# Optimization experiments

Hardware: AMD Instinct MI355X
Metric: run time of the kernel (lower is better)

## Reference

```python
import jax, jax.numpy as jnp
import numpy as np

DIM, HEADS, HD, FFN = 1536, 12, 128, 8960
B, F, H, W = 1, 4, 20, 32
S = F * H * W          # 2560 latent tokens
L2 = 512               # text context length
EPS = 1e-6


def _ln(x):
    m = jnp.mean(x, -1, keepdims=True)
    v = jnp.mean(jnp.square(x - m), -1, keepdims=True)
    return (x - m) * jax.lax.rsqrt(v + EPS)


def _rms(x, g):
    return x * jax.lax.rsqrt(jnp.mean(jnp.square(x), -1, keepdims=True) + EPS) * g


def _dyn_quant(x):
    # per-token symmetric int8 dynamic activation quantization (A8, dynamic input scale)
    s = jnp.maximum(jnp.max(jnp.abs(x), -1, keepdims=True) / 127.0, 1e-8)
    q = jnp.clip(jnp.round(x / s), -127.0, 127.0)
    return q, s, jnp.sum(q, -1)   # sum_input used for asymmetric-weight zero-point correction


def _quant_w(w):
    # per-output-channel asymmetric int8 weight quantization (weight_sym=False)
    wmin = jnp.min(w, 1, keepdims=True)
    wmax = jnp.max(w, 1, keepdims=True)
    s = jnp.maximum((wmax - wmin) / 255.0, 1e-8)
    zp = jnp.round(-128.0 - wmin / s)
    qw = jnp.clip(jnp.round(w / s) + zp, -128.0, 127.0)
    return qw, s[:, 0], zp[:, 0]


def _w8a8(qx, s_x, sum_qx, w, b):
    # y = s_x * s_w * (qx @ (qw - zp)^T) + b = s_x*s_w*(qx@qw^T - zp*sum(qx)) + b
    qw, sw, zp = _quant_w(w)
    acc = jnp.einsum('bsi,oi->bso', qx, qw) - sum_qx[..., None] * zp
    return acc * s_x * sw + b


def _rope(x, fr, f, h, w):
    # x: [B,S,N,D] with S == f*h*w; fr: [1024, D//2] complex rope table
    Bn, Sn, N, D = x.shape
    c = D // 2
    s0 = c - 2 * (c // 3)
    fF = jnp.broadcast_to(fr[:f, :s0].reshape(f, 1, 1, s0), (f, h, w, s0))
    fH = jnp.broadcast_to(fr[:h, s0:s0 + c // 3].reshape(1, h, 1, c // 3), (f, h, w, c // 3))
    fW = jnp.broadcast_to(fr[:w, s0 + c // 3:].reshape(1, 1, w, c // 3), (f, h, w, c // 3))
    fi = jnp.concatenate([fF, fH, fW], -1).reshape(1, f * h * w, 1, c)
    xr = x.reshape(Bn, Sn, N, c, 2)
    xc = jax.lax.complex(xr[..., 0], xr[..., 1]) * fi
    return jnp.stack([jnp.real(xc), jnp.imag(xc)], -1).reshape(Bn, Sn, N, D)


def _attn(q, k, v, k_lens):
    scale = 1.0 / jnp.sqrt(jnp.float32(q.shape[-1]))
    scores = jnp.einsum('bqnd,bknd->bnqk', q, k) * scale
    mask = jnp.arange(k.shape[1])[None, None, None, :] < k_lens[:, None, None, None]
    p = jax.nn.softmax(jnp.where(mask, scores, -1e30), -1)
    return jnp.einsum('bnqk,bknd->bqnd', p, v)


def _forward(x, e, freqs, context, modulation,
             wq, bq, wk, bk, wv, bv, wo, bo, gq, gk, n3_w, n3_b,
             cwq, cbq, cwk, cbk, cwv, cbv, cwo, cbo, cgq, cgk,
             w1, b1, w2, b2, f, h, w, seq_lens, context_lens):
    fr = jax.lax.complex(freqs[..., 0], freqs[..., 1])
    em = modulation + e  # [B,6,C]
    sm, sc, gm, smlp, scmlp, gmlp = [em[:, i:i + 1] for i in range(6)]
    Bn, Sn, C = x.shape
    # --- self attention: fused norm+modulation then shared per-token int8 quant for q/k/v ---
    h1 = _ln(x) * (1.0 + sc) + sm
    qx, s_x, sum_qx = _dyn_quant(h1)
    q = _rms(_w8a8(qx, s_x, sum_qx, wq, bq), gq).reshape(Bn, Sn, HEADS, HD)
    k = _rms(_w8a8(qx, s_x, sum_qx, wk, bk), gk).reshape(Bn, Sn, HEADS, HD)
    v = _w8a8(qx, s_x, sum_qx, wv, bv).reshape(Bn, Sn, HEADS, HD)
    q = _rope(q, fr, f, h, w)
    k = _rope(k, fr, f, h, w)
    y = _attn(q, k, v, seq_lens).reshape(Bn, Sn, C) @ wo.T + bo
    x = x + y * gm
    # --- cross attention (fp16/fp path in the original; use_kernel[1]=False) ---
    hx = _ln(x) * n3_w + n3_b
    cq = _rms(hx @ cwq.T + cbq, cgq).reshape(Bn, Sn, HEADS, HD)
    ck = _rms(context @ cwk.T + cbk, cgk).reshape(Bn, L2, HEADS, HD)
    cv = (context @ cwv.T + cbv).reshape(Bn, L2, HEADS, HD)
    y = _attn(cq, ck, cv, context_lens).reshape(Bn, Sn, C) @ cwo.T + cbo
    x = x + y
    # --- FFN with modulation (use_kernel[2]=False) ---
    h2 = _ln(x) * (1.0 + scmlp) + smlp
    y = jax.nn.gelu(h2 @ w1.T + b1, approximate=True) @ w2.T + b2
    return x + y * gmlp


def setup_inputs():
    key = jax.random.key(0)
    ks = jax.random.split(key, 16)

    def P(i, shape, s=0.02):
        return jax.random.normal(ks[i], shape, jnp.float32) * s

    x = jax.random.normal(ks[0], (B, S, DIM), jnp.float32)
    e = jax.random.normal(ks[1], (B, 6, DIM), jnp.float32)
    context = jax.random.normal(ks[2], (B, L2, DIM), jnp.float32)
    seq_lens = jnp.array([S], jnp.int32)
    grid_sizes = jnp.array([[F, H, W]], jnp.int32)
    context_lens = jnp.array([L2], jnp.int32)
    c = HD // 2
    pos = np.arange(1024, dtype=np.float64)[:, None]
    theta = 1.0 / (10000.0 ** (np.arange(c, dtype=np.float64) / c))
    ang = pos * theta
    freqs = jnp.asarray(np.stack([np.cos(ang), np.sin(ang)], -1), jnp.float32)
    z = lambda n: jnp.zeros((n,), jnp.float32)
    o = lambda n: jnp.ones((n,), jnp.float32)
    return dict(x=x, e=e, seq_lens=seq_lens, grid_sizes=grid_sizes, freqs=freqs,
                context=context, context_lens=context_lens,
                modulation=P(3, (1, 6, DIM), 1.0 / DIM ** 0.5),
                wq=P(4, (DIM, DIM)), bq=z(DIM), wk=P(5, (DIM, DIM)), bk=z(DIM),
                wv=P(6, (DIM, DIM)), bv=z(DIM), wo=P(7, (DIM, DIM)), bo=z(DIM),
                gq=o(DIM), gk=o(DIM), n3_w=o(DIM), n3_b=z(DIM),
                cwq=P(8, (DIM, DIM)), cbq=z(DIM), cwk=P(9, (DIM, DIM)), cbk=z(DIM),
                cwv=P(10, (DIM, DIM)), cbv=z(DIM), cwo=P(11, (DIM, DIM)), cbo=z(DIM),
                cgq=o(DIM), cgk=o(DIM),
                w1=P(12, (FFN, DIM)), b1=z(FFN), w2=P(13, (DIM, FFN)), b2=z(DIM))


def reference(x, e, seq_lens, grid_sizes, freqs, context, context_lens, modulation,
              wq, bq, wk, bk, wv, bv, wo, bo, gq, gk, n3_w, n3_b,
              cwq, cbq, cwk, cbk, cwv, cbv, cwo, cbo, cgq, cgk,
              w1, b1, w2, b2):
    f, h, w = int(grid_sizes[0, 0]), int(grid_sizes[0, 1]), int(grid_sizes[0, 2])
    return _forward(x, e, freqs, context, modulation,
                    wq, bq, wk, bk, wv, bv, wo, bo, gq, gk, n3_w, n3_b,
                    cwq, cbq, cwk, cbk, cwv, cbv, cwo, cbo, cgq, cgk,
                    w1, b1, w2, b2, f, h, w, seq_lens, context_lens)
```

## Files before the change

### kernel.cpp

```cpp
#include <hip/hip_runtime.h>
#include <stdint.h>


typedef unsigned short u16;
typedef __bf16 bf16x8 __attribute__((ext_vector_type(8)));
typedef float f32x4 __attribute__((ext_vector_type(4)));

#define DEV __device__ __forceinline__

DEV u16 f2b(float f) {
  uint32_t u = __float_as_uint(f);
  u += 0x7fffu + ((u >> 16) & 1u);
  return (u16)(u >> 16);
}

DEV float gelu_tanh(float v) {
  float u = 0.7978845608028654f * (v + 0.044715f * v * v * v);
  return 0.5f * v * (1.0f + tanhf(u));
}

DEV void gl_lds16(const u16* g, u16* l) {
  __builtin_amdgcn_global_load_lds(
      (const __attribute__((address_space(1))) void*)g,
      (__attribute__((address_space(3))) void*)l, 16, 0, 0);
}

DEV float bred_sum(float v, float* scr) {
  #pragma unroll
  for (int o = 32; o; o >>= 1) v += __shfl_down(v, o, 64);
  if ((threadIdx.x & 63) == 0) scr[threadIdx.x >> 6] = v;
  __syncthreads();
  v = scr[0] + scr[1] + scr[2] + scr[3];
  __syncthreads();
  return v;
}
DEV float bred_max(float v, float* scr) {
  #pragma unroll
  for (int o = 32; o; o >>= 1) v = fmaxf(v, __shfl_down(v, o, 64));
  if ((threadIdx.x & 63) == 0) scr[threadIdx.x >> 6] = v;
  __syncthreads();
  v = fmaxf(fmaxf(scr[0], scr[1]), fmaxf(scr[2], scr[3]));
  __syncthreads();
  return v;
}
DEV float bred_min(float v, float* scr) {
  #pragma unroll
  for (int o = 32; o; o >>= 1) v = fminf(v, __shfl_down(v, o, 64));
  if ((threadIdx.x & 63) == 0) scr[threadIdx.x >> 6] = v;
  __syncthreads();
  v = fminf(fminf(scr[0], scr[1]), fminf(scr[2], scr[3]));
  __syncthreads();
  return v;
}

__global__ __launch_bounds__(256) void pack_kernel(
    const float* __restrict__ e, const float* __restrict__ mod,
    const float* __restrict__ cbk, const float* __restrict__ cbv,
    float* __restrict__ em, float* __restrict__ bckv) {
  int i = blockIdx.x * 256 + threadIdx.x;
  if (i < 9216) em[i] = e[i] + mod[i];
  if (i < 3072) bckv[i] = (i < 1536) ? cbk[i] : cbv[i - 1536];
}

__global__ __launch_bounds__(256) void cvt_bf16_kernel(
    const float* __restrict__ in, u16* __restrict__ out, int n4) {
  int stride = gridDim.x * 256;
  for (int i = blockIdx.x * 256 + threadIdx.x; i < n4; i += stride) {
    float4 v = ((const float4*)in)[i];
    uint2 r;
    r.x = (uint32_t)f2b(v.x) | ((uint32_t)f2b(v.y) << 16);
    r.y = (uint32_t)f2b(v.z) | ((uint32_t)f2b(v.w) << 16);
    ((uint2*)out)[i] = r;
  }
}

__global__ __launch_bounds__(256) void ln_quant_kernel(
    const float* __restrict__ x, const float* __restrict__ em,
    u16* __restrict__ qx, float* __restrict__ sx, float* __restrict__ sumq) {
  __shared__ float scr[4];
  const int row = blockIdx.x, tid = threadIdx.x;
  const float* xr = x + (size_t)row * 1536;
  float v[6], s = 0.f, s2 = 0.f;
  #pragma unroll
  for (int t = 0; t < 6; t++) { v[t] = xr[tid + t * 256]; s += v[t]; s2 += v[t] * v[t]; }
  s = bred_sum(s, scr); s2 = bred_sum(s2, scr);
  float mean = s / 1536.f;
  float var = s2 / 1536.f - mean * mean;
  float inv = rsqrtf(var + 1e-6f);
  float hv[6], amax = 0.f;
  #pragma unroll
  for (int t = 0; t < 6; t++) {
    int i = tid + t * 256;
    hv[t] = (v[t] - mean) * inv * (1.f + em[1536 + i]) + em[i];
    amax = fmaxf(amax, fabsf(hv[t]));
  }
  amax = bred_max(amax, scr);
  float sxv = fmaxf(amax / 127.f, 1e-8f);
  float qs = 0.f;
  #pragma unroll
  for (int t = 0; t < 6; t++) {
    int i = tid + t * 256;
    float q = fminf(fmaxf(rintf(hv[t] / sxv), -127.f), 127.f);
    qs += q;
    qx[(size_t)row * 1536 + i] = f2b(q);
  }
  qs = bred_sum(qs, scr);
  if (tid == 0) { sx[row] = sxv; sumq[row] = qs; }
}

__global__ __launch_bounds__(256) void quantw_kernel(
    const float* __restrict__ wq, const float* __restrict__ wk, const float* __restrict__ wv,
    const float* __restrict__ bq, const float* __restrict__ bk, const float* __restrict__ bv,
    u16* __restrict__ qw, float* __restrict__ sw, float* __restrict__ zp, float* __restrict__ ball) {
  __shared__ float scr[4];
  const int row = blockIdx.x, tid = threadIdx.x;
  const int sel = (row >= 3072) ? 2 : (row >= 1536 ? 1 : 0);
  const int r = row - sel * 1536;
  const float* w = sel == 0 ? wq : (sel == 1 ? wk : wv);
  const float* bb = sel == 0 ? bq : (sel == 1 ? bk : bv);
  const float* wr = w + (size_t)r * 1536;
  float v[6], mn = 1e30f, mx = -1e30f;
  #pragma unroll
  for (int t = 0; t < 6; t++) { v[t] = wr[tid + t * 256]; mn = fminf(mn, v[t]); mx = fmaxf(mx, v[t]); }
  mn = bred_min(mn, scr); mx = bred_max(mx, scr);
  float s = fmaxf((mx - mn) / 255.f, 1e-8f);
  float z = rintf(-128.f - mn / s);
  #pragma unroll
  for (int t = 0; t < 6; t++) {
    int i = tid + t * 256;
    float q = fminf(fmaxf(rintf(v[t] / s) + z, -128.f), 127.f);
    qw[(size_t)row * 1536 + i] = f2b(q);
  }
  if (tid == 0) { sw[row] = s; zp[row] = z; ball[row] = bb[r]; }
}

template<int EP>
DEV void gemm_epilogue(float v, int row, int col, int N, void* Cout,
                       const float* bias, const float* sxp, const float* sumqp,
                       const float* swp, const float* zpp,
                       const float* gp, const float* residp) {
  size_t idx = (size_t)row * N + col;
  if constexpr (EP == 0) {
    ((float*)Cout)[idx] = v + bias[col];
  } else if constexpr (EP == 1) {
    v = (v - sumqp[row] * zpp[col]) * (sxp[row] * swp[col]) + bias[col];
    ((float*)Cout)[idx] = v;
  } else if constexpr (EP == 2) {
    v += bias[col];
    if (gp) v *= gp[col];
    ((float*)Cout)[idx] = v + residp[idx];
  } else if constexpr (EP == 3) {
    ((u16*)Cout)[idx] = f2b(gelu_tanh(v + bias[col]));
  } else {
    ((float*)Cout)[idx] = v;
  }
}

struct PtrQuad { void* p0; void* p1; void* p2; void* p3; };

template<int EP>
__global__ __launch_bounds__(512, 2) void gemm256_bt_kernel(
    const u16* __restrict__ A, const u16* __restrict__ B, PtrQuad pq,
    int N, int K, int KC,
    const float* __restrict__ bias,
    const float* __restrict__ sxp, const float* __restrict__ sumqp,
    const float* __restrict__ swp, const float* __restrict__ zpp) {
  __shared__ __align__(16) u16 As[2][256 * 64];
  __shared__ __align__(16) u16 Bs[2][256 * 64];
  const int tid = threadIdx.x;
  const int wave = tid >> 6, lane = tid & 63;
  const int wm = wave >> 2, wn = wave & 3;
  const int quad = lane >> 4, l16 = lane & 15;

  const int gx = gridDim.x, gy = gridDim.y;
  const int nwg = gx * gy * (int)gridDim.z;
  const int orig = ((int)blockIdx.z * gy + (int)blockIdx.y) * gx + (int)blockIdx.x;
  const int qq = nwg >> 3, rr = nwg & 7, xcd = orig & 7, lin = orig >> 3;
  const int wg = (xcd < rr ? xcd * (qq + 1) : rr * (qq + 1) + (xcd - rr) * qq) + lin;
  const int bx = wg % gx, t2 = wg / gx, by = t2 % gy, bz = t2 / gy;
  const int m0 = by * 256, n0 = bx * 256;

  const u16* Abase = A + (size_t)m0 * K + (size_t)bz * KC;
  const u16* Bbase = B + (size_t)n0 * K + (size_t)bz * KC;

  const u16* ap[4]; const u16* bp[4];
  #pragma unroll
  for (int i = 0; i < 4; i++) {
    int idx = i * 512 + tid;
    int row = idx >> 3;
    int col = ((idx & 7) ^ (row & 7)) * 8;
    ap[i] = Abase + (size_t)row * K + col;
    bp[i] = Bbase + (size_t)row * K + col;
  }

  f32x4 acc[8][4];
  #pragma unroll
  for (int i = 0; i < 8; i++)
    #pragma unroll
    for (int j = 0; j < 4; j++) acc[i][j] = (f32x4){0.f, 0.f, 0.f, 0.f};

  auto stA = [&](int buf, int kt) {
    #pragma unroll
    for (int i = 0; i < 4; i++)
      gl_lds16(ap[i] + (kt << 6), &As[buf][(i * 512 + wave * 64) * 8]);
  };
  auto stB = [&](int buf, int kt) {
    #pragma unroll
    for (int i = 0; i < 4; i++)
      gl_lds16(bp[i] + (kt << 6), &Bs[buf][(i * 512 + wave * 64) * 8]);
  };

  bf16x8 afr[4][2], bfr[2][2];
  auto ldA = [&](int cur, int mh) {
    #pragma unroll
    for (int f = 0; f < 4; f++) {
      int row = wm * 128 + mh * 64 + f * 16 + l16;
      int rx = row & 7;
      #pragma unroll
      for (int kk = 0; kk < 2; kk++)
        afr[f][kk] = *(const bf16x8*)&As[cur][row * 64 + (((kk * 4 + quad) ^ rx) << 3)];
    }
  };
  auto ldB = [&](int cur, int nh) {
    #pragma unroll
    for (int f = 0; f < 2; f++) {
      int row = wn * 64 + nh * 32 + f * 16 + l16;
      int rx = row & 7;
      #pragma unroll
      for (int kk = 0; kk < 2; kk++)
        bfr[f][kk] = *(const bf16x8*)&Bs[cur][row * 64 + (((kk * 4 + quad) ^ rx) << 3)];
    }
  };
  auto mmaQ = [&](int mh, int nh) {
    __builtin_amdgcn_s_setprio(1);
    #pragma unroll
    for (int kk = 0; kk < 2; kk++)
      #pragma unroll
      for (int f = 0; f < 4; f++)
        #pragma unroll
        for (int g = 0; g < 2; g++)
          acc[mh * 4 + f][nh * 2 + g] = __builtin_amdgcn_mfma_f32_16x16x32_bf16(
              afr[f][kk], bfr[g][kk], acc[mh * 4 + f][nh * 2 + g], 0, 0, 0);
    __builtin_amdgcn_s_setprio(0);
  };

  const int nk = KC >> 6;
  stA(0, 0); stB(0, 0);
  asm volatile("s_waitcnt vmcnt(0)" ::: "memory");
  __builtin_amdgcn_s_barrier();

  for (int kt = 0; kt < nk; kt++) {
    const int cur = kt & 1, nxt = cur ^ 1;
    const bool pf = (kt + 1 < nk);
    ldA(cur, 0); ldB(cur, 0);
    if (pf) stA(nxt, kt + 1);
    __builtin_amdgcn_s_barrier();
    mmaQ(0, 0);
    __builtin_amdgcn_s_barrier();
    ldB(cur, 1);
    if (pf) stB(nxt, kt + 1);
    __builtin_amdgcn_s_barrier();
    mmaQ(0, 1);
    __builtin_amdgcn_s_barrier();
    ldA(cur, 1);
    __builtin_amdgcn_s_barrier();
    mmaQ(1, 1);
    __builtin_amdgcn_s_barrier();
    ldB(cur, 0);
    __builtin_amdgcn_s_barrier();
    mmaQ(1, 0);
    if (pf) asm volatile("s_waitcnt vmcnt(0)" ::: "memory");
    __builtin_amdgcn_s_barrier();
  }

  void* Cuse;
  if constexpr (EP == 4)
    Cuse = bz == 0 ? pq.p0 : (bz == 1 ? pq.p1 : (bz == 2 ? pq.p2 : pq.p3));
  else
    Cuse = pq.p0;
  #pragma unroll
  for (int mi = 0; mi < 8; mi++)
    #pragma unroll
    for (int ni = 0; ni < 4; ni++) {
      int col = n0 + wn * 64 + ni * 16 + l16;
      #pragma unroll
      for (int r = 0; r < 4; r++)
        gemm_epilogue<EP>(acc[mi][ni][r], m0 + wm * 128 + mi * 16 + quad * 4 + r, col,
                          N, Cuse, bias, sxp, sumqp, swp, zpp, nullptr, nullptr);
    }
}

template<int EP>
__global__ __launch_bounds__(256) void gemm64_bt_kernel(
    const u16* __restrict__ A, const u16* __restrict__ B,
    void* __restrict__ Cout, void* __restrict__ Cout2, int N, int K, int KC,
    const float* __restrict__ bias,
    const float* __restrict__ sxp, const float* __restrict__ sumqp,
    const float* __restrict__ swp, const float* __restrict__ zpp,
    const float* __restrict__ gp, const float* __restrict__ residp) {
  __shared__ __align__(16) u16 As[2][64 * 64];
  __shared__ __align__(16) u16 Bs[2][128 * 64];
  const int tid = threadIdx.x;
  const int wave = tid >> 6, lane = tid & 63;
  const int wm = wave >> 1, wn = wave & 1;
  const int quad = lane >> 4, l16 = lane & 15;
  const int m0 = blockIdx.y * 64, n0 = blockIdx.x * 128;
  const int kstart = blockIdx.z * KC;

  int arow[2], acol[2], brow[4], bcol[4];
  #pragma unroll
  for (int i = 0; i < 2; i++) {
    int row = (wave * 2 + i) * 8 + (lane >> 3);
    arow[i] = row; acol[i] = (((lane & 7) - (row >> 1)) & 7) * 8;
  }
  #pragma unroll
  for (int i = 0; i < 4; i++) {
    int row = (wave * 4 + i) * 8 + (lane >> 3);
    brow[i] = row; bcol[i] = (((lane & 7) - (row >> 1)) & 7) * 8;
  }

  f32x4 acc[2][4];
  #pragma unroll
  for (int i = 0; i < 2; i++)
    #pragma unroll
    for (int j = 0; j < 4; j++) acc[i][j] = (f32x4){0.f, 0.f, 0.f, 0.f};

  const int nk = KC >> 6;
  auto stage = [&](int buf, int k0) {
    #pragma unroll
    for (int i = 0; i < 2; i++)
      gl_lds16(A + (size_t)(m0 + arow[i]) * K + kstart + k0 + acol[i],
               &As[buf][(wave * 2 + i) * 512]);
    #pragma unroll
    for (int i = 0; i < 4; i++)
      gl_lds16(B + (size_t)(n0 + brow[i]) * K + kstart + k0 + bcol[i],
               &Bs[buf][(wave * 4 + i) * 512]);
  };
  stage(0, 0);
  for (int kt = 0; kt < nk; kt++) {
    __syncthreads();
    const int cur = kt & 1;
    if (kt + 1 < nk) stage(1 - cur, (kt + 1) << 6);
    #pragma unroll
    for (int s = 0; s < 2; s++) {
      bf16x8 af[2], bfv[4];
      #pragma unroll
      for (int mi = 0; mi < 2; mi++) {
        int row = wm * 32 + mi * 16 + l16;
        int slot = ((s * 4 + quad) + (row >> 1)) & 7;
        af[mi] = *(const bf16x8*)&As[cur][row * 64 + slot * 8];
      }
      #pragma unroll
      for (int ni = 0; ni < 4; ni++) {
        int row = wn * 64 + ni * 16 + l16;
        int slot = ((s * 4 + quad) + (row >> 1)) & 7;
        bfv[ni] = *(const bf16x8*)&Bs[cur][row * 64 + slot * 8];
      }
      #pragma unroll
      for (int mi = 0; mi < 2; mi++)
        #pragma unroll
        for (int ni = 0; ni < 4; ni++)
          acc[mi][ni] = __builtin_amdgcn_mfma_f32_16x16x32_bf16(af[mi], bfv[ni], acc[mi][ni], 0, 0, 0);
    }
  }
  void* Cuse = (EP == 4 && blockIdx.z) ? Cout2 : Cout;
  #pragma unroll
  for (int mi = 0; mi < 2; mi++)
    #pragma unroll
    for (int ni = 0; ni < 4; ni++) {
      int col = n0 + wn * 64 + ni * 16 + l16;
      #pragma unroll
      for (int r = 0; r < 4; r++)
        gemm_epilogue<EP>(acc[mi][ni][r], m0 + wm * 32 + mi * 16 + quad * 4 + r, col,
                          N, Cuse, bias, sxp, sumqp, swp, zpp, gp, residp);
    }
}

__global__ __launch_bounds__(256) void splitk_reduce4_kernel(
    const float* __restrict__ P0, const float* __restrict__ P1,
    const float* __restrict__ P2, const float* __restrict__ P3,
    float* __restrict__ out, const float* __restrict__ bias,
    const float* __restrict__ g, const float* __restrict__ resid,
    int N, int n4) {
  int stride = gridDim.x * 256;
  for (int i = blockIdx.x * 256 + threadIdx.x; i < n4; i += stride) {
    float4 a = ((const float4*)P0)[i];
    float4 b = ((const float4*)P1)[i];
    float4 c = ((const float4*)P2)[i];
    float4 d = ((const float4*)P3)[i];
    float4 r = ((const float4*)resid)[i];
    int col = (i * 4) % N;
    float4 o;
    o.x = (a.x + b.x + c.x + d.x + bias[col]) * g[col] + r.x;
    o.y = (a.y + b.y + c.y + d.y + bias[col + 1]) * g[col + 1] + r.y;
    o.z = (a.z + b.z + c.z + d.z + bias[col + 2]) * g[col + 2] + r.z;
    o.w = (a.w + b.w + c.w + d.w + bias[col + 3]) * g[col + 3] + r.w;
    ((float4*)out)[i] = o;
  }
}

__global__ __launch_bounds__(256) void rmsrope_b_kernel(
    const float* __restrict__ qkv, u16* __restrict__ qkvb,
    const float* __restrict__ gq, const float* __restrict__ gk,
    const float* __restrict__ freqs, const int* __restrict__ gsz) {
  __shared__ float scr[4];
  const int row = blockIdx.x, tid = threadIdx.x;
  const float* base = qkv + (size_t)row * 4608;
  u16* ob = qkvb + (size_t)row * 4608;
  const int gh = gsz[1], gw = gsz[2];
  const int hw = gh * gw;
  const int fi = row / hw, rem = row - fi * hw;
  const int hi = rem / gw, wi = rem - hi * gw;
  #pragma unroll
  for (int part = 0; part < 2; part++) {
    const float* p = base + part * 1536;
    u16* o = ob + part * 1536;
    const float* g = part ? gk : gq;
    const float sc = part ? 1.f : 0.08838834764831845f;
    float v[6], s2 = 0.f;
    #pragma unroll
    for (int t = 0; t < 6; t++) { v[t] = p[tid + t * 256]; s2 += v[t] * v[t]; }
    s2 = bred_sum(s2, scr);
    float inv = rsqrtf(s2 / 1536.f + 1e-6f);
    #pragma unroll
    for (int t = 0; t < 3; t++) {
      int pr = tid + t * 256;
      int c = pr & 63;
      int frow = (c < 22) ? fi : (c < 43 ? hi : wi);
      const float* fr = freqs + ((size_t)frow * 64 + c) * 2;
      float cv = fr[0], sv = fr[1];
      float x0 = p[2 * pr] * inv * g[2 * pr];
      float x1 = p[2 * pr + 1] * inv * g[2 * pr + 1];
      o[2 * pr] = f2b((x0 * cv - x1 * sv) * sc);
      o[2 * pr + 1] = f2b((x0 * sv + x1 * cv) * sc);
    }
  }
  #pragma unroll
  for (int t = 0; t < 6; t++) {
    int i = tid + t * 256;
    ob[3072 + i] = f2b(base[3072 + i]);
  }
}

__global__ __launch_bounds__(256) void rms_bf16_kernel(
    const float* __restrict__ X, u16* __restrict__ O, const float* __restrict__ g,
    int ldi, int ldo, float scale) {
  __shared__ float scr[4];
  const int row = blockIdx.x, tid = threadIdx.x;
  const float* xr = X + (size_t)row * ldi;
  u16* orow = O + (size_t)row * ldo;
  float v[6], s2 = 0.f;
  #pragma unroll
  for (int t = 0; t < 6; t++) { v[t] = xr[tid + t * 256]; s2 += v[t] * v[t]; }
  s2 = bred_sum(s2, scr);
  float inv = rsqrtf(s2 / 1536.f + 1e-6f) * scale;
  #pragma unroll
  for (int t = 0; t < 6; t++) {
    int i = tid + t * 256;
    orow[i] = f2b(v[t] * inv * g[i]);
  }
}

__global__ __launch_bounds__(256) void vtrans_kernel(
    const float* __restrict__ V, int ld, u16* __restrict__ Vt, int Skv) {
  __shared__ u16 T[64 * 136];
  const int h = blockIdx.y, k0 = blockIdx.x * 64, tid = threadIdx.x;
  #pragma unroll
  for (int i = 0; i < 8; i++) {
    int f4 = i * 256 + tid;
    int row = f4 >> 5, c4 = f4 & 31;
    float4 v = *(const float4*)(V + (size_t)(k0 + row) * ld + h * 128 + c4 * 4);
    ushort4 b;
    b.x = f2b(v.x); b.y = f2b(v.y); b.z = f2b(v.z); b.w = f2b(v.w);
    *(ushort4*)&T[row * 136 + c4 * 4] = b;
  }
  __syncthreads();
  #pragma unroll
  for (int i = 0; i < 4; i++) {
    int f8 = i * 256 + tid;
    int hd = f8 >> 3, kc = f8 & 7;
    u16 tmp[8];
    #pragma unroll
    for (int j = 0; j < 8; j++) tmp[j] = T[(kc * 8 + j) * 136 + hd];
    *(uint4*)(Vt + ((size_t)h * 128 + hd) * Skv + k0 + kc * 8) = *(const uint4*)tmp;
  }
}

__global__ __launch_bounds__(256) void fattn_kernel(
    const u16* __restrict__ Q, int ldq, const u16* __restrict__ Kg, int ldk,
    const u16* __restrict__ Vtg, u16* __restrict__ O, int ldo,
    const int* __restrict__ klen_ptr, int kmax) {
  __shared__ __align__(16) u16 Qs[64 * 136];
  __shared__ __align__(16) u16 Ks[64 * 136];
  __shared__ __align__(16) u16 Vt[128 * 72];
  __shared__ __align__(16) u16 Pt[4][16 * 72];
  const int tid = threadIdx.x, wave = tid >> 6, lane = tid & 63;
  const int quad = lane >> 4, l16 = lane & 15;
  const int h = blockIdx.y;
  const int q0 = blockIdx.x * 64;
  int klen = klen_ptr[0]; if (klen > kmax) klen = kmax;
  const u16* vbase = Vtg + (size_t)h * 128 * kmax;

  #pragma unroll
  for (int i = 0; i < 4; i++) {
    int c8 = i * 256 + tid;
    int row = c8 >> 4, cc = (c8 & 15) * 8;
    *(uint4*)&Qs[row * 136 + cc] = *(const uint4*)(Q + (size_t)(q0 + row) * ldq + h * 128 + cc);
  }
  __syncthreads();
  bf16x8 qf[4];
  #pragma unroll
  for (int s = 0; s < 4; s++)
    qf[s] = *(const bf16x8*)&Qs[(wave * 16 + l16) * 136 + s * 32 + quad * 8];

  float m_r[4] = {-1e30f, -1e30f, -1e30f, -1e30f};
  float l_r[4] = {0.f, 0.f, 0.f, 0.f};
  f32x4 oacc[8];
  #pragma unroll
  for (int n8 = 0; n8 < 8; n8++) oacc[n8] = (f32x4){0.f, 0.f, 0.f, 0.f};

  const int ktiles = (klen + 63) >> 6;
  for (int kt = 0; kt < ktiles; kt++) {
    const int k0 = kt * 64;
    __syncthreads();
    #pragma unroll
    for (int i = 0; i < 4; i++) {
      int c8 = i * 256 + tid;
      int row = c8 >> 4, cc = (c8 & 15) * 8;
      *(uint4*)&Ks[row * 136 + cc] = *(const uint4*)(Kg + (size_t)(k0 + row) * ldk + h * 128 + cc);
    }
    #pragma unroll
    for (int i = 0; i < 4; i++) {
      int f8 = i * 256 + tid;
      int hd = f8 >> 3, kc = f8 & 7;
      *(uint4*)&Vt[hd * 72 + kc * 8] = *(const uint4*)(vbase + (size_t)hd * kmax + k0 + kc * 8);
    }
    __syncthreads();
    f32x4 sacc[4];
    #pragma unroll
    for (int ni = 0; ni < 4; ni++) sacc[ni] = (f32x4){0.f, 0.f, 0.f, 0.f};
    #pragma unroll
    for (int ni = 0; ni < 4; ni++)
      #pragma unroll
      for (int s = 0; s < 4; s++) {
        bf16x8 kf = *(const bf16x8*)&Ks[(ni * 16 + l16) * 136 + s * 32 + quad * 8];
        sacc[ni] = __builtin_amdgcn_mfma_f32_16x16x32_bf16(qf[s], kf, sacc[ni], 0, 0, 0);
      }
    float alpha_r[4];
    #pragma unroll
    for (int r = 0; r < 4; r++) {
      float mx = -1e30f;
      #pragma unroll
      for (int ni = 0; ni < 4; ni++) {
        int col = k0 + ni * 16 + l16;
        float sv = (col < klen) ? sacc[ni][r] : -1e30f;
        sacc[ni][r] = sv;
        mx = fmaxf(mx, sv);
      }
      #pragma unroll
      for (int off = 1; off < 16; off <<= 1) mx = fmaxf(mx, __shfl_xor(mx, off, 64));
      float mnew = fmaxf(m_r[r], mx);
      float alpha = __expf(m_r[r] - mnew);
      float rsum = 0.f;
      float pv[4];
      #pragma unroll
      for (int ni = 0; ni < 4; ni++) {
        float p = __expf(sacc[ni][r] - mnew);
        pv[ni] = p;
        rsum += p;
      }
      #pragma unroll
      for (int off = 1; off < 16; off <<= 1) rsum += __shfl_xor(rsum, off, 64);
      l_r[r] = l_r[r] * alpha + rsum;
      m_r[r] = mnew;
      alpha_r[r] = alpha;
      #pragma unroll
      for (int ni = 0; ni < 4; ni++)
        Pt[wave][(quad * 4 + r) * 72 + ni * 16 + l16] = f2b(pv[ni]);
    }
    #pragma unroll
    for (int n8 = 0; n8 < 8; n8++)
      #pragma unroll
      for (int r = 0; r < 4; r++) oacc[n8][r] *= alpha_r[r];
    #pragma unroll
    for (int s2 = 0; s2 < 2; s2++) {
      bf16x8 pf = *(const bf16x8*)&Pt[wave][l16 * 72 + s2 * 32 + quad * 8];
      #pragma unroll
      for (int n8 = 0; n8 < 8; n8++) {
        bf16x8 vf = *(const bf16x8*)&Vt[(n8 * 16 + l16) * 72 + s2 * 32 + quad * 8];
        oacc[n8] = __builtin_amdgcn_mfma_f32_16x16x32_bf16(pf, vf, oacc[n8], 0, 0, 0);
      }
    }
  }
  float rl[4];
  #pragma unroll
  for (int r = 0; r < 4; r++) rl[r] = 1.f / l_r[r];
  #pragma unroll
  for (int n8 = 0; n8 < 8; n8++)
    #pragma unroll
    for (int r = 0; r < 4; r++) {
      int row = q0 + wave * 16 + quad * 4 + r;
      O[(size_t)row * ldo + h * 128 + n8 * 16 + l16] = f2b(oacc[n8][r] * rl[r]);
    }
}

__global__ __launch_bounds__(256) void ln_affine_kernel(
    const float* __restrict__ X, u16* __restrict__ O,
    const float* __restrict__ w, const float* __restrict__ b, float addone) {
  __shared__ float scr[4];
  const int row = blockIdx.x, tid = threadIdx.x;
  const float* xr = X + (size_t)row * 1536;
  float v[6], s = 0.f, s2 = 0.f;
  #pragma unroll
  for (int t = 0; t < 6; t++) { v[t] = xr[tid + t * 256]; s += v[t]; s2 += v[t] * v[t]; }
  s = bred_sum(s, scr); s2 = bred_sum(s2, scr);
  float mean = s / 1536.f;
  float inv = rsqrtf(s2 / 1536.f - mean * mean + 1e-6f);
  #pragma unroll
  for (int t = 0; t < 6; t++) {
    int i = tid + t * 256;
    O[(size_t)row * 1536 + i] = f2b((v[t] - mean) * inv * (addone + w[i]) + b[i]);
  }
}

extern "C" void kernel_launch(void* const* d_in, const int* in_sizes, int n_in,
                              void* d_out, int out_size, void* d_ws, size_t ws_size,
                              hipStream_t stream) {
  (void)in_sizes; (void)n_in; (void)out_size; (void)ws_size;
  const int S = 2560, D = 1536, L2C = 512, FF = 8960, ND = 4608, CKV = 3072;

  const float* x = (const float*)d_in[0];
  const float* e = (const float*)d_in[1];
  const int* seq_lens = (const int*)d_in[2];
  const int* grid_sz = (const int*)d_in[3];
  const float* freqs = (const float*)d_in[4];
  const float* context = (const float*)d_in[5];
  const int* ctx_lens = (const int*)d_in[6];
  const float* modulation = (const float*)d_in[7];
  const float* wq = (const float*)d_in[8];  const float* bq = (const float*)d_in[9];
  const float* wk = (const float*)d_in[10]; const float* bk = (const float*)d_in[11];
  const float* wv = (const float*)d_in[12]; const float* bv = (const float*)d_in[13];
  const float* wo = (const float*)d_in[14]; const float* bo = (const float*)d_in[15];
  const float* gq = (const float*)d_in[16]; const float* gk = (const float*)d_in[17];
  const float* n3w = (const float*)d_in[18]; const float* n3b = (const float*)d_in[19];
  const float* cwq = (const float*)d_in[20]; const float* cbq = (const float*)d_in[21];
  const float* cwk = (const float*)d_in[22]; const float* cbk = (const float*)d_in[23];
  const float* cwv = (const float*)d_in[24]; const float* cbv = (const float*)d_in[25];
  const float* cwo = (const float*)d_in[26]; const float* cbo = (const float*)d_in[27];
  const float* cgq = (const float*)d_in[28]; const float* cgk = (const float*)d_in[29];
  const float* w1 = (const float*)d_in[30]; const float* b1 = (const float*)d_in[31];
  const float* w2 = (const float*)d_in[32]; const float* b2 = (const float*)d_in[33];

  char* wsb = (char*)d_ws;
  size_t off = 0;
  auto alloc = [&](size_t bytes) -> void* {
    void* r = wsb + off;
    off += (bytes + 255) & ~(size_t)255;
    return r;
  };
  float* em   = (float*)alloc((size_t)6 * D * 4);
  float* bckv = (float*)alloc((size_t)CKV * 4);
  float* ball = (float*)alloc((size_t)ND * 4);
  float* sx   = (float*)alloc((size_t)S * 4);
  float* sumq = (float*)alloc((size_t)S * 4);
  float* sw   = (float*)alloc((size_t)ND * 4);
  float* zp   = (float*)alloc((size_t)ND * 4);
  u16* qx     = (u16*)alloc((size_t)S * D * 2);
  u16* qw     = (u16*)alloc((size_t)ND * D * 2);
  float* qkv  = (float*)alloc((size_t)S * ND * 4);
  u16* qkvb   = (u16*)alloc((size_t)S * ND * 2);
  u16* attnb  = (u16*)alloc((size_t)S * D * 2);
  u16* hx     = (u16*)alloc((size_t)S * D * 2);
  float* cq   = (float*)alloc((size_t)S * D * 4);
  float* ckv  = (float*)alloc((size_t)L2C * CKV * 4);
  u16* ctxb   = (u16*)alloc((size_t)L2C * D * 2);
  u16* cattn  = (u16*)alloc((size_t)S * D * 2);
  u16* wo_b   = (u16*)alloc((size_t)D * D * 2);
  u16* cwq_b  = (u16*)alloc((size_t)D * D * 2);
  u16* cwkv_b = (u16*)alloc((size_t)2 * D * D * 2);
  u16* cwo_b  = (u16*)alloc((size_t)D * D * 2);
  u16* w1_b   = (u16*)alloc((size_t)FF * D * 2);
  u16* w2_b   = (u16*)alloc((size_t)D * FF * 2);
  u16* h3 = (u16*)qkv;
  u16* h2 = attnb;
  u16* vtg = qw;
  u16* cvtg = qx;
  u16* cqb = hx;
  u16* ckvb = ctxb;
  float* x2 = cq;
  float* x1 = (float*)d_out;
  float* outp = (float*)d_out;
  float* P0 = (float*)qx;
  float* P1 = (float*)qkvb;
  float* P2 = (float*)attnb;
  float* P3 = (float*)cattn;

  auto cvt = [&](const float* in, u16* op, size_t n) {
    int n4 = (int)(n / 4);
    int blocks = (n4 + 255) / 256; if (blocks > 4096) blocks = 4096;
    cvt_bf16_kernel<<<blocks, 256, 0, stream>>>(in, op, n4);
  };

  pack_kernel<<<36, 256, 0, stream>>>(e, modulation, cbk, cbv, em, bckv);
  cvt(wo, wo_b, (size_t)D * D);
  cvt(cwq, cwq_b, (size_t)D * D);
  cvt(cwk, cwkv_b, (size_t)D * D);
  cvt(cwv, cwkv_b + (size_t)D * D, (size_t)D * D);
  cvt(cwo, cwo_b, (size_t)D * D);
  cvt(w1, w1_b, (size_t)FF * D);
  cvt(w2, w2_b, (size_t)D * FF);
  cvt(context, ctxb, (size_t)L2C * D);

  ln_quant_kernel<<<S, 256, 0, stream>>>(x, em, qx, sx, sumq);
  quantw_kernel<<<ND, 256, 0, stream>>>(wq, wk, wv, bq, bk, bv, qw, sw, zp, ball);

  {
    PtrQuad pq{qkv, nullptr, nullptr, nullptr};
    gemm256_bt_kernel<1><<<dim3(ND / 256, S / 256), 512, 0, stream>>>(
        qx, qw, pq, ND, D, D, ball, sx, sumq, sw, zp);
  }

  rmsrope_b_kernel<<<S, 256, 0, stream>>>(qkv, qkvb, gq, gk, freqs, grid_sz);
  vtrans_kernel<<<dim3(S / 64, 12), 256, 0, stream>>>(qkv + 3072, ND, vtg, S);

  fattn_kernel<<<dim3(S / 64, 12), 256, 0, stream>>>(
      qkvb, ND, qkvb + 1536, ND, vtg, attnb, D, seq_lens, S);

  gemm64_bt_kernel<2><<<dim3(D / 128, S / 64), 256, 0, stream>>>(
      attnb, wo_b, x1, nullptr, D, D, D, bo, nullptr, nullptr, nullptr, nullptr, em + 2 * D, x);

  ln_affine_kernel<<<S, 256, 0, stream>>>(x1, hx, n3w, n3b, 0.f);

  gemm64_bt_kernel<0><<<dim3(D / 128, S / 64), 256, 0, stream>>>(
      hx, cwq_b, cq, nullptr, D, D, D, cbq, nullptr, nullptr, nullptr, nullptr, nullptr, nullptr);
  gemm64_bt_kernel<0><<<dim3(CKV / 128, L2C / 64), 256, 0, stream>>>(
      ctxb, cwkv_b, ckv, nullptr, CKV, D, D, bckv, nullptr, nullptr, nullptr, nullptr, nullptr, nullptr);

  rms_bf16_kernel<<<S, 256, 0, stream>>>(cq, cqb, cgq, D, D, 0.08838834764831845f);
  rms_bf16_kernel<<<L2C, 256, 0, stream>>>(ckv, ckvb, cgk, CKV, D, 1.f);
  vtrans_kernel<<<dim3(L2C / 64, 12), 256, 0, stream>>>(ckv + 1536, CKV, cvtg, L2C);

  fattn_kernel<<<dim3(S / 64, 12), 256, 0, stream>>>(
      cqb, D, ckvb, D, cvtg, cattn, D, ctx_lens, L2C);

  gemm64_bt_kernel<2><<<dim3(D / 128, S / 64), 256, 0, stream>>>(
      cattn, cwo_b, x2, nullptr, D, D, D, cbo, nullptr, nullptr, nullptr, nullptr, nullptr, x1);

  ln_affine_kernel<<<S, 256, 0, stream>>>(x2, h2, em + 4 * D, em + 3 * D, 1.f);

  {
    PtrQuad pq{h3, nullptr, nullptr, nullptr};
    gemm256_bt_kernel<3><<<dim3(FF / 256, S / 256), 512, 0, stream>>>(
        h2, w1_b, pq, FF, D, D, b1, nullptr, nullptr, nullptr, nullptr);
  }

  {
    PtrQuad pq{P0, P1, P2, P3};
    gemm256_bt_kernel<4><<<dim3(D / 256, S / 256, 4), 512, 0, stream>>>(
        h3, w2_b, pq, D, FF, FF / 4, nullptr, nullptr, nullptr, nullptr, nullptr);
  }
  splitk_reduce4_kernel<<<960, 256, 0, stream>>>(
      P0, P1, P2, P3, outp, b2, em + 5 * D, x2, D, S * D / 4);
}
```

Before: 908.5 us.

## Deepen GEMM global-to-LDS prefetch to two stages ahead and simplify GELU

Both GEMM kernels now prefetch the tile two k-steps ahead into the buffer just consumed, using partial vmcnt waits instead of draining all loads each iteration. The second GEMM loads all LDS fragments first, then issues the next prefetch, and runs the MFMAs at raised priority. This is meant to hide global-load latency behind compute. GELU's tanh form is rewritten as an equivalent sigmoid using __expf, which is cheaper but slightly less precise. The vmcnt counts are hard-coded to the number of loads per stage, so any change to the staging code would silently break the synchronisation.

```diff
diff --git a/kernel.cpp b/kernel.cpp
--- a/kernel.cpp
+++ b/kernel.cpp
@@ -7,6 +7,13 @@
 typedef float f32x4 __attribute__((ext_vector_type(4)));
 
 #define DEV __device__ __forceinline__
+
+#define WAIT_LGKM0 do { \
+  asm volatile("s_waitcnt lgkmcnt(0)" ::: "memory"); \
+  __builtin_amdgcn_sched_barrier(0); } while (0)
+#define WAIT_VM(N) do { \
+  asm volatile("s_waitcnt vmcnt(" #N ")" ::: "memory"); \
+  __builtin_amdgcn_sched_barrier(0); } while (0)
 
 DEV u16 f2b(float f) {
   uint32_t u = __float_as_uint(f);
@@ -15,8 +22,8 @@
 }
 
 DEV float gelu_tanh(float v) {
-  float u = 0.7978845608028654f * (v + 0.044715f * v * v * v);
-  return 0.5f * v * (1.0f + tanhf(u));
+  float u = 1.5957691216057308f * (v + 0.044715f * v * v * v);
+  return v / (1.f + __expf(-u));
 }
 
 DEV void gl_lds16(const u16* g, u16* l) {
@@ -246,30 +253,39 @@
 
   const int nk = KC >> 6;
   stA(0, 0); stB(0, 0);
-  asm volatile("s_waitcnt vmcnt(0)" ::: "memory");
+  if (nk > 1) {
+    stA(1, 1); stB(1, 1);
+    WAIT_VM(8);
+  } else {
+    WAIT_VM(0);
+  }
   __builtin_amdgcn_s_barrier();
 
   for (int kt = 0; kt < nk; kt++) {
-    const int cur = kt & 1, nxt = cur ^ 1;
-    const bool pf = (kt + 1 < nk);
+    const int cur = kt & 1;
+    const bool st2 = (kt + 2 < nk);
     ldA(cur, 0); ldB(cur, 0);
-    if (pf) stA(nxt, kt + 1);
     __builtin_amdgcn_s_barrier();
     mmaQ(0, 0);
     __builtin_amdgcn_s_barrier();
     ldB(cur, 1);
-    if (pf) stB(nxt, kt + 1);
     __builtin_amdgcn_s_barrier();
     mmaQ(0, 1);
     __builtin_amdgcn_s_barrier();
     ldA(cur, 1);
-    __builtin_amdgcn_s_barrier();
+    WAIT_LGKM0;
+    __builtin_amdgcn_s_barrier();
+    if (st2) stA(cur, kt + 2);
     mmaQ(1, 1);
     __builtin_amdgcn_s_barrier();
     ldB(cur, 0);
-    __builtin_amdgcn_s_barrier();
+    WAIT_LGKM0;
+    __builtin_amdgcn_s_barrier();
+    if (st2) stB(cur, kt + 2);
     mmaQ(1, 0);
-    if (pf) asm volatile("s_waitcnt vmcnt(0)" ::: "memory");
+    if (kt + 1 < nk) {
+      if (st2) { WAIT_VM(8); } else { WAIT_VM(0); }
+    }
     __builtin_amdgcn_s_barrier();
   }
 
@@ -337,31 +353,49 @@
                &Bs[buf][(wave * 4 + i) * 512]);
   };
   stage(0, 0);
+  if (nk > 1) {
+    stage(1, 64);
+    WAIT_VM(6);
+  } else {
+    WAIT_VM(0);
+  }
+  __builtin_amdgcn_s_barrier();
+
   for (int kt = 0; kt < nk; kt++) {
-    __syncthreads();
     const int cur = kt & 1;
-    if (kt + 1 < nk) stage(1 - cur, (kt + 1) << 6);
+    const bool st2 = (kt + 2 < nk);
+    bf16x8 af[2][2], bfv[2][4];
     #pragma unroll
     for (int s = 0; s < 2; s++) {
-      bf16x8 af[2], bfv[4];
       #pragma unroll
       for (int mi = 0; mi < 2; mi++) {
         int row = wm * 32 + mi * 16 + l16;
         int slot = ((s * 4 + quad) + (row >> 1)) & 7;
-        af[mi] = *(const bf16x8*)&As[cur][row * 64 + slot * 8];
+        af[s][mi] = *(const bf16x8*)&As[cur][row * 64 + slot * 8];
       }
       #pragma unroll
       for (int ni = 0; ni < 4; ni++) {
         int row = wn * 64 + ni * 16 + l16;
         int slot = ((s * 4 + quad) + (row >> 1)) & 7;
-        bfv[ni] = *(const bf16x8*)&Bs[cur][row * 64 + slot * 8];
+        bfv[s][ni] = *(const bf16x8*)&Bs[cur][row * 64 + slot * 8];
       }
+    }
+    WAIT_LGKM0;
+    __builtin_amdgcn_s_barrier();
+    if (st2) stage(cur, (kt + 2) << 6);
+    __builtin_amdgcn_s_setprio(1);
+    #pragma unroll
+    for (int s = 0; s < 2; s++)
       #pragma unroll
       for (int mi = 0; mi < 2; mi++)
         #pragma unroll
         for (int ni = 0; ni < 4; ni++)
-          acc[mi][ni] = __builtin_amdgcn_mfma_f32_16x16x32_bf16(af[mi], bfv[ni], acc[mi][ni], 0, 0, 0);
-    }
+          acc[mi][ni] = __builtin_amdgcn_mfma_f32_16x16x32_bf16(af[s][mi], bfv[s][ni], acc[mi][ni], 0, 0, 0);
+    __builtin_amdgcn_s_setprio(0);
+    if (kt + 1 < nk) {
+      if (st2) { WAIT_VM(6); } else { WAIT_VM(0); }
+    }
+    __builtin_amdgcn_s_barrier();
   }
   void* Cuse = (EP == 4 && blockIdx.z) ? Cout2 : Cout;
   #pragma unroll
```

After: 881.3 us. 3.0% less time.
